# Kernel tuning notes

Measured on AMD Instinct MI355X. Metric: run time of the kernel, lower is better.

## Reference

```python
import jax, jax.numpy as jnp
import numpy as np

N = 100000   # mesh points
n = 32       # latent dim
K = 32       # neighbours per point
M = 16       # clusters
MU = 1.0


def setup_inputs() -> dict:
    key = jax.random.key(0)
    ks = jax.random.split(key, 8)
    x = jax.random.normal(ks[0], (N,), jnp.float32)
    enc_w = jax.random.normal(ks[1], (n, N), jnp.float32) * 0.01
    enc_b = jnp.zeros((n,), jnp.float32)
    decoder = jax.random.normal(ks[2], (n, N), jnp.float32) * 0.02
    bw_w = jax.random.normal(ks[3], (n * M, n), jnp.float32) * 0.05
    bw_b = jnp.ones((n * M,), jnp.float32)  # keep bandwidths away from 0
    neighbour_distance = jax.random.uniform(ks[4], (N, K), jnp.float32, minval=0.05, maxval=1.0)
    neighbour_id = jax.random.randint(ks[5], (N, K), 0, N)
    clustering_labels = jax.random.randint(ks[6], (N,), 0, M)
    return {
        "x": x, "enc_w": enc_w, "enc_b": enc_b, "decoder": decoder,
        "bw_w": bw_w, "bw_b": bw_b,
        "neighbour_distance": neighbour_distance,
        "neighbour_id": neighbour_id,
        "clustering_labels": clustering_labels,
    }


def reference(x, enc_w, enc_b, decoder, bw_w, bw_b,
              neighbour_distance, neighbour_id, clustering_labels):
    # encode: Linear(N -> n) on a single vector
    encoded = enc_w @ x + enc_b                             # [n]
    # per-(basis, cluster) bandwidths, broadcast to points via labels
    bandwidths = (bw_w @ encoded + bw_b).reshape(n, M)      # [n, M]
    w = bandwidths[:, clustering_labels]                    # [n, N]
    # bubble window: relu(1 - d^2 / (w*mu)^2), shape [n, N, K]
    window = jax.nn.relu(1.0 - neighbour_distance[None, :, :] ** 2
                         / (w[:, :, None] * MU) ** 2)
    # NOTE: original normalizes over dim=1 (the N-points axis) — faithful here
    window = window / jnp.sum(window, axis=1, keepdims=True)
    # gather decoder rows at neighbours and reduce over neighbour axis
    convolved = jnp.sum(decoder[:, neighbour_id] * window, axis=-1)  # [n, N]
    return encoded @ convolved                              # [N]
```

## Files before the change

### kernel.cpp

```cpp
#include <hip/hip_runtime.h>

#define NPTS 100000

constexpr int IB1  = 128;
constexpr int SPB2 = 1536;
constexpr int GTB  = 3125;

typedef _Float16 half_t;
typedef _Float16 half4 __attribute__((ext_vector_type(4)));

constexpr size_t OFF_PART   = 0;
constexpr size_t OFF_ENC    = 32768;
constexpr size_t OFF_INVW2  = 33024;
constexpr size_t OFF_SACC   = 35072;
constexpr size_t OFF_SPARTF = 43264;
constexpr size_t OFF_GTH    = 6334720;

__global__ __launch_bounds__(256) void k_enc_partial(
    const float* __restrict__ x, const float* __restrict__ enc_w,
    double* __restrict__ part, double* __restrict__ Sacc) {
  int tid = threadIdx.x;
  if (blockIdx.x == 0) {
    for (int q = tid; q < 1024; q += 256) Sacc[q] = 0.0;
  }
  int jg = blockIdx.x & 3;
  int ib = blockIdx.x >> 2;
  int j0 = jg * 8;
  double acc[8];
#pragma unroll
  for (int jj = 0; jj < 8; ++jj) acc[jj] = 0.0;
  for (int i = ib * 256 + tid; i < NPTS; i += IB1 * 256) {
    float xv = x[i];
#pragma unroll
    for (int jj = 0; jj < 8; ++jj)
      acc[jj] += (double)enc_w[(size_t)(j0 + jj) * NPTS + i] * (double)xv;
  }
#pragma unroll
  for (int jj = 0; jj < 8; ++jj) {
    double v = acc[jj];
#pragma unroll
    for (int off = 32; off >= 1; off >>= 1) v += __shfl_down(v, off);
    acc[jj] = v;
  }
  __shared__ double sw[4][8];
  int lane = tid & 63, w = tid >> 6;
  if (lane == 0)
    for (int jj = 0; jj < 8; ++jj) sw[w][jj] = acc[jj];
  __syncthreads();
  if (tid < 8) {
    double s = sw[0][tid] + sw[1][tid] + sw[2][tid] + sw[3][tid];
    part[(size_t)(j0 + tid) * IB1 + ib] = s;
  }
}

__global__ __launch_bounds__(512) void k_head(
    const double* __restrict__ part, const float* __restrict__ enc_b,
    const float* __restrict__ bw_w, const float* __restrict__ bw_b,
    double* __restrict__ enc_out, float* __restrict__ invw2) {
  __shared__ double es[32];
  __shared__ double sred[32][16];
  int tid = threadIdx.x;
  int j = tid >> 4, slot = tid & 15;
  double s = 0.0;
#pragma unroll
  for (int r = 0; r < 8; ++r) s += part[j * 128 + slot * 8 + r];
  sred[j][slot] = s;
  __syncthreads();
  if (tid < 32) {
    double t = 0.0;
    for (int q = 0; q < 16; ++q) t += sred[tid][q];
    t += (double)enc_b[tid];
    enc_out[tid] = t;
    es[tid] = t;
  }
  __syncthreads();
  double wd = 0.0;
  for (int c = 0; c < 32; ++c) wd += (double)bw_w[tid * 32 + c] * es[c];
  wd += (double)bw_b[tid];
  int jr = tid >> 4, m = tid & 15;
  invw2[m * 32 + jr] = (float)(1.0 / (wd * wd));
}

__global__ __launch_bounds__(256) void k_gtspart(
    const float* __restrict__ decoder, const double* __restrict__ enc,
    const float* __restrict__ nd, const int* __restrict__ labels,
    const float* __restrict__ invw2_g, float* __restrict__ spartf,
    half_t* __restrict__ gTh) {
  int tid = threadIdx.x;
  int b = blockIdx.x;
  if (b < SPB2) {
    __shared__ float iw[512];
    for (int q = tid; q < 512; q += 256) iw[q] = invw2_g[q];
    __syncthreads();
    int j = tid >> 3, kq = tid & 7;
    float t0 = 0.0f, t1 = 0.0f, t2 = 0.0f, t3 = 0.0f;
    int cnt = (NPTS - b + SPB2 - 1) / SPB2;
#pragma unroll 4
    for (int c = 0; c < cnt; ++c) {
      int i = b + c * SPB2;
      int lab = labels[i];
      float icv = iw[lab * 32 + j];
      float4 d = *(const float4*)&nd[(size_t)i * 32 + kq * 4];
      t0 += fmaxf(fmaf(-(d.x * d.x), icv, 1.0f), 0.0f);
      t1 += fmaxf(fmaf(-(d.y * d.y), icv, 1.0f), 0.0f);
      t2 += fmaxf(fmaf(-(d.z * d.z), icv, 1.0f), 0.0f);
      t3 += fmaxf(fmaf(-(d.w * d.w), icv, 1.0f), 0.0f);
    }
    float4 v = make_float4(t0, t1, t2, t3);
    *(float4*)&spartf[(size_t)b * 1024 + j * 32 + kq * 4] = v;
  } else {
    __shared__ float tile[32][33];
    __shared__ float ef[32];
    int gb = b - SPB2;
    if (tid < 32) ef[tid] = (float)enc[tid];
    int tx = tid & 31, ty = tid >> 5;
    int i0 = gb * 32;
    for (int jj = ty; jj < 32; jj += 8)
      tile[tx][jj] = decoder[(size_t)jj * NPTS + i0 + tx];
    __syncthreads();
    for (int ii = ty; ii < 32; ii += 8)
      gTh[(size_t)(i0 + ii) * 32 + tx] = (half_t)(tile[ii][tx] * ef[tx]);
  }
}

__global__ __launch_bounds__(256) void k_sred(
    const float* __restrict__ spartf, double* __restrict__ Sacc) {
  int gt = blockIdx.x * 256 + threadIdx.x;
  int jk = gt & 1023;
  int seg = gt >> 10;
  double s = 0.0;
#pragma unroll 8
  for (int r = 0; r < SPB2 / 16; ++r)
    s += (double)spartf[(size_t)(seg * (SPB2 / 16) + r) * 1024 + jk];
  unsafeAtomicAdd(&Sacc[jk], s);
}

__global__ __launch_bounds__(256, 4) void k_main(
    const float* __restrict__ nd, const int* __restrict__ nid,
    const int* __restrict__ labels, const half_t* __restrict__ gTh,
    const float* __restrict__ invw2_g, const double* __restrict__ Sacc,
    float* __restrict__ out) {
  __shared__ __align__(16) float iwL[512];
  __shared__ __align__(16) float isL[1024];
  int tid = threadIdx.x;
#pragma unroll
  for (int u = 0; u < 2; ++u) iwL[tid + 256 * u] = invw2_g[tid + 256 * u];
#pragma unroll
  for (int u = 0; u < 4; ++u) {
    int t = tid * 4 + u;
    int j = t >> 5, k = t & 31;
    isL[k * 32 + j] = 1.0f / (float)Sacc[t];
  }
  __syncthreads();
  int lane = tid & 63;
  int w = tid >> 6;
  int q = lane & 7;
  int g = lane >> 3;
  int wv = blockIdx.x * 4 + w;

  int id[4][4];
  float dvv[4][4];
  int lab[4];
#pragma unroll
  for (int p = 0; p < 4; ++p) {
    int i = wv + p * 25000;
    lab[p] = labels[i];
    int base = i * 32;
#pragma unroll
    for (int kk = 0; kk < 4; ++kk) {
      id[p][kk] = nid[base + kk * 8 + g];
      dvv[p][kk] = nd[base + kk * 8 + g];
    }
  }
  half4 gv[4][4];
#pragma unroll
  for (int p = 0; p < 4; ++p)
#pragma unroll
    for (int kk = 0; kk < 4; ++kk)
      gv[p][kk] = *(const half4*)&gTh[(size_t)id[p][kk] * 32 + q * 4];
  float4 iwv[4];
#pragma unroll
  for (int p = 0; p < 4; ++p)
    iwv[p] = *(const float4*)&iwL[lab[p] * 32 + q * 4];
  float4 sv[4];
#pragma unroll
  for (int kk = 0; kk < 4; ++kk)
    sv[kk] = *(const float4*)&isL[(kk * 8 + g) * 32 + q * 4];

  double a[4];
#pragma unroll
  for (int p = 0; p < 4; ++p) {
    float ap = 0.0f;
#pragma unroll
    for (int kk = 0; kk < 4; ++kk) {
      float md = -dvv[p][kk] * dvv[p][kk];
      float u0 = fmaxf(fmaf(md, iwv[p].x, 1.0f), 0.0f);
      float u1 = fmaxf(fmaf(md, iwv[p].y, 1.0f), 0.0f);
      float u2 = fmaxf(fmaf(md, iwv[p].z, 1.0f), 0.0f);
      float u3 = fmaxf(fmaf(md, iwv[p].w, 1.0f), 0.0f);
      ap += (float)gv[p][kk].x * (u0 * sv[kk].x);
      ap += (float)gv[p][kk].y * (u1 * sv[kk].y);
      ap += (float)gv[p][kk].z * (u2 * sv[kk].z);
      ap += (float)gv[p][kk].w * (u3 * sv[kk].w);
    }
    a[p] = (double)ap;
  }
#pragma unroll
  for (int off = 32; off >= 1; off >>= 1) {
#pragma unroll
    for (int p = 0; p < 4; ++p) a[p] += __shfl_down(a[p], off);
  }
  if (lane == 0) {
#pragma unroll
    for (int p = 0; p < 4; ++p) out[wv + p * 25000] = (float)a[p];
  }
}

extern "C" void kernel_launch(void* const* d_in, const int* in_sizes, int n_in,
                              void* d_out, int out_size, void* d_ws,
                              size_t ws_size, hipStream_t stream) {
  const float* x       = (const float*)d_in[0];
  const float* enc_w   = (const float*)d_in[1];
  const float* enc_b   = (const float*)d_in[2];
  const float* decoder = (const float*)d_in[3];
  const float* bw_w    = (const float*)d_in[4];
  const float* bw_b    = (const float*)d_in[5];
  const float* nd      = (const float*)d_in[6];
  const int*   nid     = (const int*)d_in[7];
  const int*   labels  = (const int*)d_in[8];
  float* out = (float*)d_out;

  char* ws = (char*)d_ws;
  double* part   = (double*)(ws + OFF_PART);
  double* enc_d  = (double*)(ws + OFF_ENC);
  float*  invw2  = (float*)(ws + OFF_INVW2);
  double* Sacc   = (double*)(ws + OFF_SACC);
  float*  spartf = (float*)(ws + OFF_SPARTF);
  half_t* gTh    = (half_t*)(ws + OFF_GTH);

  hipLaunchKernelGGL(k_enc_partial, dim3(512), dim3(256), 0, stream,
                     x, enc_w, part, Sacc);
  hipLaunchKernelGGL(k_head, dim3(1), dim3(512), 0, stream,
                     part, enc_b, bw_w, bw_b, enc_d, invw2);
  hipLaunchKernelGGL(k_gtspart, dim3(SPB2 + GTB), dim3(256), 0, stream,
                     decoder, enc_d, nd, labels, invw2, spartf, gTh);
  hipLaunchKernelGGL(k_sred, dim3(64), dim3(256), 0, stream, spartf, Sacc);
  hipLaunchKernelGGL(k_main, dim3(6250), dim3(256), 0, stream,
                     nd, nid, labels, gTh, invw2, Sacc, out);
}
```

Before: 161.3 us.

## Split gather table into two latent halves processed by separate main passes

The fp16 gathered decoder table is split into two 16-column tables, each 3.2MB, so each pass's random-gather working set is smaller and more likely to stay cache-resident. The main kernel runs twice, once per half; the first pass writes partial outputs and the second adds them. Streaming inputs (enc_w, decoder, labels, neighbour arrays) are now read with nontemporal loads to avoid polluting cache. In exchange, the neighbour ids, distances and labels are read twice and an extra launch plus partial-output round trip is added.

```diff
diff --git a/kernel.cpp b/kernel.cpp
--- a/kernel.cpp
+++ b/kernel.cpp
@@ -14,7 +14,9 @@
 constexpr size_t OFF_INVW2  = 33024;
 constexpr size_t OFF_SACC   = 35072;
 constexpr size_t OFF_SPARTF = 43264;
-constexpr size_t OFF_GTH    = 6334720;
+constexpr size_t OFF_GTH0   = 6334720;
+constexpr size_t OFF_GTH1   = 9534720;
+constexpr size_t OFF_OPART  = 12734720;
 
 __global__ __launch_bounds__(256) void k_enc_partial(
     const float* __restrict__ x, const float* __restrict__ enc_w,
@@ -32,8 +34,10 @@
   for (int i = ib * 256 + tid; i < NPTS; i += IB1 * 256) {
     float xv = x[i];
 #pragma unroll
-    for (int jj = 0; jj < 8; ++jj)
-      acc[jj] += (double)enc_w[(size_t)(j0 + jj) * NPTS + i] * (double)xv;
+    for (int jj = 0; jj < 8; ++jj) {
+      float wv = __builtin_nontemporal_load(&enc_w[(size_t)(j0 + jj) * NPTS + i]);
+      acc[jj] += (double)wv * (double)xv;
+    }
   }
 #pragma unroll
   for (int jj = 0; jj < 8; ++jj) {
@@ -85,7 +89,7 @@
     const float* __restrict__ decoder, const double* __restrict__ enc,
     const float* __restrict__ nd, const int* __restrict__ labels,
     const float* __restrict__ invw2_g, float* __restrict__ spartf,
-    half_t* __restrict__ gTh) {
+    half_t* __restrict__ gTh0, half_t* __restrict__ gTh1) {
   int tid = threadIdx.x;
   int b = blockIdx.x;
   if (b < SPB2) {
@@ -98,7 +102,7 @@
 #pragma unroll 4
     for (int c = 0; c < cnt; ++c) {
       int i = b + c * SPB2;
-      int lab = labels[i];
+      int lab = __builtin_nontemporal_load(&labels[i]);
       float icv = iw[lab * 32 + j];
       float4 d = *(const float4*)&nd[(size_t)i * 32 + kq * 4];
       t0 += fmaxf(fmaf(-(d.x * d.x), icv, 1.0f), 0.0f);
@@ -116,10 +120,12 @@
     int tx = tid & 31, ty = tid >> 5;
     int i0 = gb * 32;
     for (int jj = ty; jj < 32; jj += 8)
-      tile[tx][jj] = decoder[(size_t)jj * NPTS + i0 + tx];
+      tile[tx][jj] = __builtin_nontemporal_load(&decoder[(size_t)jj * NPTS + i0 + tx]);
     __syncthreads();
+    half_t* tab = (tx < 16) ? gTh0 : gTh1;
+    int jx = tx & 15;
     for (int ii = ty; ii < 32; ii += 8)
-      gTh[(size_t)(i0 + ii) * 32 + tx] = (half_t)(tile[ii][tx] * ef[tx]);
+      tab[(size_t)(i0 + ii) * 16 + jx] = (half_t)(tile[ii][tx] * ef[tx]);
   }
 }
 
@@ -135,64 +141,66 @@
   unsafeAtomicAdd(&Sacc[jk], s);
 }
 
-__global__ __launch_bounds__(256, 4) void k_main(
+template <int PASS>
+__global__ __launch_bounds__(256, 4) void k_main_half(
     const float* __restrict__ nd, const int* __restrict__ nid,
-    const int* __restrict__ labels, const half_t* __restrict__ gTh,
+    const int* __restrict__ labels, const half_t* __restrict__ tab,
     const float* __restrict__ invw2_g, const double* __restrict__ Sacc,
-    float* __restrict__ out) {
+    float* __restrict__ opart, float* __restrict__ out) {
+  const int h16 = PASS * 16;
   __shared__ __align__(16) float iwL[512];
-  __shared__ __align__(16) float isL[1024];
+  __shared__ __align__(16) float isL[512];
   int tid = threadIdx.x;
 #pragma unroll
   for (int u = 0; u < 2; ++u) iwL[tid + 256 * u] = invw2_g[tid + 256 * u];
 #pragma unroll
-  for (int u = 0; u < 4; ++u) {
-    int t = tid * 4 + u;
-    int j = t >> 5, k = t & 31;
-    isL[k * 32 + j] = 1.0f / (float)Sacc[t];
+  for (int u = 0; u < 2; ++u) {
+    int t = tid * 2 + u;
+    int k = t >> 4, jj = t & 15;
+    isL[k * 16 + jj] = 1.0f / (float)Sacc[(h16 + jj) * 32 + k];
   }
   __syncthreads();
   int lane = tid & 63;
   int w = tid >> 6;
-  int q = lane & 7;
-  int g = lane >> 3;
+  int q = lane & 3;
+  int g = lane >> 2;
   int wv = blockIdx.x * 4 + w;
 
-  int id[4][4];
-  float dvv[4][4];
+  int id[4][2];
+  float dvv[4][2];
   int lab[4];
 #pragma unroll
   for (int p = 0; p < 4; ++p) {
     int i = wv + p * 25000;
-    lab[p] = labels[i];
+    lab[p] = __builtin_nontemporal_load(&labels[i]);
     int base = i * 32;
 #pragma unroll
-    for (int kk = 0; kk < 4; ++kk) {
-      id[p][kk] = nid[base + kk * 8 + g];
-      dvv[p][kk] = nd[base + kk * 8 + g];
-    }
-  }
-  half4 gv[4][4];
+    for (int kk = 0; kk < 2; ++kk) {
+      id[p][kk] = __builtin_nontemporal_load(&nid[base + kk * 16 + g]);
+      dvv[p][kk] = __builtin_nontemporal_load(&nd[base + kk * 16 + g]);
+    }
+  }
+  half4 gv[4][2];
 #pragma unroll
   for (int p = 0; p < 4; ++p)
 #pragma unroll
-    for (int kk = 0; kk < 4; ++kk)
-      gv[p][kk] = *(const half4*)&gTh[(size_t)id[p][kk] * 32 + q * 4];
+    for (int kk = 0; kk < 2; ++kk)
+      gv[p][kk] = *(const half4*)&tab[(size_t)id[p][kk] * 16 + q * 4];
   float4 iwv[4];
 #pragma unroll
   for (int p = 0; p < 4; ++p)
-    iwv[p] = *(const float4*)&iwL[lab[p] * 32 + q * 4];
-  float4 sv[4];
-#pragma unroll
-  for (int kk = 0; kk < 4; ++kk)
-    sv[kk] = *(const float4*)&isL[(kk * 8 + g) * 32 + q * 4];
+    iwv[p] = *(const float4*)&iwL[lab[p] * 32 + h16 + q * 4];
+  float4 sv[2];
+#pragma unroll
+  for (int kk = 0; kk < 2; ++kk)
+    sv[kk] = *(const float4*)&isL[(kk * 16 + g) * 16 + q * 4];
 
   double a[4];
 #pragma unroll
   for (int p = 0; p < 4; ++p) {
     float ap = 0.0f;
 #pragma unroll
-    for (int kk = 0; kk < 4; ++kk) {
+    for (int kk = 0; kk < 2; ++kk) {
       float md = -dvv[p][kk] * dvv[p][kk];
       float u0 = fmaxf(fmaf(md, iwv[p].x, 1.0f), 0.0f);
       float u1 = fmaxf(fmaf(md, iwv[p].y, 1.0f), 0.0f);
@@ -212,7 +220,14 @@
   }
   if (lane == 0) {
 #pragma unroll
-    for (int p = 0; p < 4; ++p) out[wv + p * 25000] = (float)a[p];
+    for (int p = 0; p < 4; ++p) {
+      int i = wv + p * 25000;
+      if (PASS == 0) {
+        __builtin_nontemporal_store((float)a[p], &opart[i]);
+      } else {
+        out[i] = opart[i] + (float)a[p];
+      }
+    }
   }
 }
 
@@ -236,15 +251,19 @@
   float*  invw2  = (float*)(ws + OFF_INVW2);
   double* Sacc   = (double*)(ws + OFF_SACC);
   float*  spartf = (float*)(ws + OFF_SPARTF);
-  half_t* gTh    = (half_t*)(ws + OFF_GTH);
+  half_t* gTh0   = (half_t*)(ws + OFF_GTH0);
+  half_t* gTh1   = (half_t*)(ws + OFF_GTH1);
+  float*  opart  = (float*)(ws + OFF_OPART);
 
   hipLaunchKernelGGL(k_enc_partial, dim3(512), dim3(256), 0, stream,
                      x, enc_w, part, Sacc);
   hipLaunchKernelGGL(k_head, dim3(1), dim3(512), 0, stream,
                      part, enc_b, bw_w, bw_b, enc_d, invw2);
   hipLaunchKernelGGL(k_gtspart, dim3(SPB2 + GTB), dim3(256), 0, stream,
-                     decoder, enc_d, nd, labels, invw2, spartf, gTh);
+                     decoder, enc_d, nd, labels, invw2, spartf, gTh0, gTh1);
   hipLaunchKernelGGL(k_sred, dim3(64), dim3(256), 0, stream, spartf, Sacc);
-  hipLaunchKernelGGL(k_main, dim3(6250), dim3(256), 0, stream,
-                     nd, nid, labels, gTh, invw2, Sacc, out);
-}
+  hipLaunchKernelGGL((k_main_half<0>), dim3(6250), dim3(256), 0, stream,
+                     nd, nid, labels, gTh0, invw2, Sacc, opart, out);
+  hipLaunchKernelGGL((k_main_half<1>), dim3(6250), dim3(256), 0, stream,
+                     nd, nid, labels, gTh1, invw2, Sacc, opart, out);
+}
```

Measured after the change: 196.4 us. 1.22x slower.
